# Kernel tuning notes

Hardware: AMD Instinct MI355X
Metric: run time of the kernel (lower is better)

Reference implementation:

```python
import jax, jax.numpy as jnp
import numpy as np

B, SQ, SK, DK, DV = 8, 2048, 2048, 256, 256
EPS = 1e-7  # keras.backend.epsilon()


def setup_inputs() -> dict:
    key = jax.random.key(0)
    kq, kk, kv, km = jax.random.split(key, 4)
    query = jax.random.normal(kq, (B, SQ, DK), dtype=jnp.float32)
    k_ = jax.random.normal(kk, (B, SK, DK), dtype=jnp.float32)
    value = jax.random.normal(kv, (B, SK, DV), dtype=jnp.float32)
    mask = jax.random.uniform(km, (B, SK)) > 0.1
    return {"query": query, "key": k_, "value": value, "mask": mask}


def reference(query, key, value, mask):
    d = query.shape[-1]
    # scores: [B, Sq, Sk]
    e = jnp.einsum('bqd,bkd->bqk', query, key) / jnp.sqrt(jnp.asarray(d, query.dtype))
    # original applies exp(e - max) BEFORE masking (non-standard but faithful)
    e = jnp.exp(e - jnp.max(e, axis=-1, keepdims=True))
    q_len, k_len = query.shape[1], key.shape[1]
    causal = (jnp.arange(k_len)[None, :] <= jnp.arange(q_len)[:, None]).astype(query.dtype)
    e = e * causal[None, :, :]                       # history_only mask
    e = e * mask[:, None, :].astype(query.dtype)     # key padding mask
    a = e / (jnp.sum(e, axis=-1, keepdims=True) + EPS)
    return jnp.einsum('bqk,bkv->bqv', a, value)
```

## Files before the change

### kernel.cpp

```cpp
#include <hip/hip_runtime.h>
#include <hip/hip_bf16.h>

#define B_   8
#define SQ_  2048
#define SK_  2048
#define DK_  256
#define DV_  256

#define KT    32
#define PSTR  40
#define TELEM (KT * DK_)
#define NQB   16

typedef __bf16 bf16x8 __attribute__((ext_vector_type(8)));
typedef float  f32x4  __attribute__((ext_vector_type(4)));

__device__ __forceinline__ void gl_lds16(const void* g, void* l) {
    __builtin_amdgcn_global_load_lds(
        (const __attribute__((address_space(1))) void*)g,
        (__attribute__((address_space(3))) void*)l, 16, 0, 0);
}

__global__ __launch_bounds__(256)
void make_tiles(const float* __restrict__ K, const float* __restrict__ V,
                __bf16* __restrict__ Kt, __bf16* __restrict__ Vt)
{
    const int b = blockIdx.x, t = blockIdx.y;
    {
        __bf16* out = Kt + ((size_t)(b * 64 + t)) * TELEM;
        const float* src = K + ((size_t)(b * SK_ + t * KT)) * DK_;
        #pragma unroll
        for (int it = 0; it < 4; ++it) {
            int ci  = it * 256 + threadIdx.x;
            int dk8 = ci >> 5;
            int key = ci & 31;
            const float* p = src + (size_t)key * DK_ + dk8 * 8;
            float4 f0 = *(const float4*)(p);
            float4 f1 = *(const float4*)(p + 4);
            bf16x8 o;
            o[0] = (__bf16)f0.x; o[1] = (__bf16)f0.y; o[2] = (__bf16)f0.z; o[3] = (__bf16)f0.w;
            o[4] = (__bf16)f1.x; o[5] = (__bf16)f1.y; o[6] = (__bf16)f1.z; o[7] = (__bf16)f1.w;
            *(bf16x8*)(out + (size_t)ci * 8) = o;
        }
    }
    {
        __bf16* out = Vt + ((size_t)(b * 64 + t)) * TELEM;
        const float* src = V + ((size_t)(b * SK_ + t * KT)) * DV_;
        int kc8 = threadIdx.x >> 6;
        int dv4 = threadIdx.x & 63;
        const float* p = src + (size_t)(kc8 * 8) * DV_ + dv4 * 4;
        bf16x8 o0, o1, o2, o3;
        #pragma unroll
        for (int j = 0; j < 8; ++j) {
            float4 f = *(const float4*)(p + (size_t)j * DV_);
            o0[j] = (__bf16)f.x; o1[j] = (__bf16)f.y;
            o2[j] = (__bf16)f.z; o3[j] = (__bf16)f.w;
        }
        __bf16* q = out + (size_t)(kc8 * 256 + dv4 * 4) * 8;
        *(bf16x8*)(q)      = o0;
        *(bf16x8*)(q + 8)  = o1;
        *(bf16x8*)(q + 16) = o2;
        *(bf16x8*)(q + 24) = o3;
    }
}

__global__ __launch_bounds__(256, 2)
void attn_fwd(const float* __restrict__ Qg, const __bf16* __restrict__ Kt,
              const __bf16* __restrict__ Vt, const void* __restrict__ Mv,
              __bf16* __restrict__ Opart, float* __restrict__ Lpart,
              int tpc, int slotcap)
{
    __shared__ __align__(16) __bf16 sK[2][TELEM];
    __shared__ __align__(16) __bf16 sV[2][TELEM];
    __shared__ __align__(16) __bf16 sP[4][32 * PSTR];

    const int tid  = threadIdx.x;
    const int wv   = tid >> 6;
    const int lane = tid & 63;
    const int quad = lane >> 4;
    const int l16  = lane & 15;

    const int b = blockIdx.x;

    int yy = blockIdx.y, qb = 0, s = 0;
    for (int q = NQB - 1; q >= 0; --q) {
        int c = (4 * (q + 1) + tpc - 1) / tpc;
        if (yy < c) { qb = q; s = yy; break; }
        yy -= c;
    }
    const int nt = 4 * (qb + 1);
    const int nc = (nt + tpc - 1) / tpc;
    const int t0 = nt * s / nc;
    const int t1 = nt * (s + 1) / nc;

    const int qrow = qb * 128 + wv * 32;

    const unsigned char* Mb = (const unsigned char*)Mv;
    const int*           Mi = (const int*)Mv;
    int nzb = 0;
    {
        const unsigned int* mw = (const unsigned int*)Mv;
        #pragma unroll
        for (int i = 0; i < 32; ++i) {
            unsigned int w = mw[i];
            nzb += ((w & 0x000000ffu) != 0) + ((w & 0x0000ff00u) != 0)
                 + ((w & 0x00ff0000u) != 0) + ((w & 0xff000000u) != 0);
        }
    }
    const bool mask_byte = (nzb > 40);

    bf16x8 qfrag[2][8];
    #pragma unroll
    for (int rs = 0; rs < 2; ++rs) {
        const float* qp = Qg + ((size_t)(b * SQ_ + qrow + rs * 16 + l16)) * DK_ + quad * 8;
        #pragma unroll
        for (int kt = 0; kt < 8; ++kt) {
            float4 f0 = *(const float4*)(qp + kt * 32);
            float4 f1 = *(const float4*)(qp + kt * 32 + 4);
            bf16x8 q;
            q[0] = (__bf16)f0.x; q[1] = (__bf16)f0.y; q[2] = (__bf16)f0.z; q[3] = (__bf16)f0.w;
            q[4] = (__bf16)f1.x; q[5] = (__bf16)f1.y; q[6] = (__bf16)f1.z; q[7] = (__bf16)f1.w;
            qfrag[rs][kt] = q;
        }
    }

    f32x4 oacc[2][16];
    #pragma unroll
    for (int rs = 0; rs < 2; ++rs)
        #pragma unroll
        for (int v = 0; v < 16; ++v) oacc[rs][v] = (f32x4){0.f, 0.f, 0.f, 0.f};
    float lsum[2][4] = {{0.f,0.f,0.f,0.f},{0.f,0.f,0.f,0.f}};

    const __bf16* Kbase = Kt + (size_t)b * 64 * TELEM;
    const __bf16* Vbase = Vt + (size_t)b * 64 * TELEM;
    const size_t  mbase = (size_t)b * SK_;

    {
        const __bf16* kg = Kbase + (size_t)t0 * TELEM;
        const __bf16* vg = Vbase + (size_t)t0 * TELEM;
        #pragma unroll
        for (int r = 0; r < 4; ++r) {
            int ci = r * 256 + tid;
            gl_lds16(kg + (size_t)ci * 8, (char*)&sK[0][0] + ci * 16);
            gl_lds16(vg + (size_t)ci * 8, (char*)&sV[0][0] + ci * 16);
        }
    }
    __syncthreads();

    int cur = 0;
    for (int t = t0; t < t1; ++t) {
        if (t + 1 < t1) {
            const __bf16* kg = Kbase + (size_t)(t + 1) * TELEM;
            const __bf16* vg = Vbase + (size_t)(t + 1) * TELEM;
            #pragma unroll
            for (int r = 0; r < 4; ++r) {
                int ci = r * 256 + tid;
                gl_lds16(kg + (size_t)ci * 8, (char*)&sK[cur ^ 1][0] + ci * 16);
                gl_lds16(vg + (size_t)ci * 8, (char*)&sV[cur ^ 1][0] + ci * 16);
            }
        }

        const int k0 = t * KT;

        f32x4 s00 = {0.f,0.f,0.f,0.f}, s01 = {0.f,0.f,0.f,0.f};
        f32x4 s10 = {0.f,0.f,0.f,0.f}, s11 = {0.f,0.f,0.f,0.f};
        #pragma unroll
        for (int kt = 0; kt < 8; ++kt) {
            bf16x8 b0 = *(const bf16x8*)&sK[cur][(size_t)((kt * 4 + quad) * 32 + l16)      * 8];
            bf16x8 b1 = *(const bf16x8*)&sK[cur][(size_t)((kt * 4 + quad) * 32 + 16 + l16) * 8];
            s00 = __builtin_amdgcn_mfma_f32_16x16x32_bf16(qfrag[0][kt], b0, s00, 0, 0, 0);
            s01 = __builtin_amdgcn_mfma_f32_16x16x32_bf16(qfrag[0][kt], b1, s01, 0, 0, 0);
            s10 = __builtin_amdgcn_mfma_f32_16x16x32_bf16(qfrag[1][kt], b0, s10, 0, 0, 0);
            s11 = __builtin_amdgcn_mfma_f32_16x16x32_bf16(qfrag[1][kt], b1, s11, 0, 0, 0);
        }

        #pragma unroll
        for (int nf = 0; nf < 2; ++nf) {
            int key = k0 + nf * 16 + l16;
            float mk = mask_byte ? (Mb[mbase + key] ? 1.0f : 0.0f)
                                 : (Mi[mbase + key] ? 1.0f : 0.0f);
            #pragma unroll
            for (int rs = 0; rs < 2; ++rs) {
                f32x4 sv = (rs == 0) ? ((nf == 0) ? s00 : s01)
                                     : ((nf == 0) ? s10 : s11);
                #pragma unroll
                for (int i = 0; i < 4; ++i) {
                    int qr = qrow + rs * 16 + quad * 4 + i;
                    float p = __expf(sv[i] * 0.0625f);
                    p = (key <= qr) ? (p * mk) : 0.0f;
                    lsum[rs][i] += p;
                    sP[wv][(rs * 16 + quad * 4 + i) * PSTR + nf * 16 + l16] = (__bf16)p;
                }
            }
        }
        asm volatile("s_waitcnt lgkmcnt(0)" ::: "memory");
        __builtin_amdgcn_wave_barrier();

        {
            bf16x8 pa0 = *(const bf16x8*)&sP[wv][(l16)      * PSTR + quad * 8];
            bf16x8 pa1 = *(const bf16x8*)&sP[wv][(16 + l16) * PSTR + quad * 8];
            #pragma unroll
            for (int vf = 0; vf < 16; ++vf) {
                bf16x8 bv = *(const bf16x8*)&sV[cur][(size_t)(quad * 256 + vf * 16 + l16) * 8];
                oacc[0][vf] = __builtin_amdgcn_mfma_f32_16x16x32_bf16(pa0, bv, oacc[0][vf], 0, 0, 0);
                oacc[1][vf] = __builtin_amdgcn_mfma_f32_16x16x32_bf16(pa1, bv, oacc[1][vf], 0, 0, 0);
            }
        }

        __syncthreads();
        cur ^= 1;
    }

    const size_t slot = ((size_t)(b * NQB + qb)) * slotcap + s;
    #pragma unroll
    for (int rs = 0; rs < 2; ++rs)
        #pragma unroll
        for (int i = 0; i < 4; ++i) {
            float v = lsum[rs][i];
            v += __shfl_xor(v, 1);
            v += __shfl_xor(v, 2);
            v += __shfl_xor(v, 4);
            v += __shfl_xor(v, 8);
            lsum[rs][i] = v;
        }
    if (l16 == 0) {
        #pragma unroll
        for (int rs = 0; rs < 2; ++rs)
            #pragma unroll
            for (int i = 0; i < 4; ++i)
                Lpart[slot * 128 + wv * 32 + rs * 16 + quad * 4 + i] = lsum[rs][i];
    }
    __bf16* ob = Opart + slot * (size_t)(128 * 256);
    #pragma unroll
    for (int rs = 0; rs < 2; ++rs)
        #pragma unroll
        for (int vf = 0; vf < 16; ++vf)
            #pragma unroll
            for (int i = 0; i < 4; ++i)
                ob[(wv * 32 + rs * 16 + quad * 4 + i) * 256 + vf * 16 + l16]
                    = (__bf16)oacc[rs][vf][i];
}

__global__ __launch_bounds__(512)
void attn_reduce(const __bf16* __restrict__ Opart, const float* __restrict__ Lpart,
                 float* __restrict__ Og, int tpc, int slotcap)
{
    const int b    = blockIdx.x;
    const int y    = blockIdx.y;
    const int qb64 = y >> 1;
    const int half = y & 1;
    const int qb   = qb64 >> 1;
    const int rowbase = (qb64 & 1) * 64;
    const int nt   = 4 * (qb + 1);
    const int chunks = (nt + tpc - 1) / tpc;
    const int tid  = threadIdx.x;
    const int row  = tid >> 3;
    const int cg   = tid & 7;

    const size_t sbase = ((size_t)(b * NQB + qb)) * slotcap;
    float acc[16];
    #pragma unroll
    for (int i = 0; i < 16; ++i) acc[i] = 0.f;
    float ls = 0.f;

    for (int s = 0; s < chunks; ++s) {
        const __bf16* p = Opart + (sbase + s) * (size_t)(128 * 256)
                        + (size_t)(rowbase + row) * 256 + half * 128 + cg * 16;
        bf16x8 x0 = *(const bf16x8*)(p);
        bf16x8 x1 = *(const bf16x8*)(p + 8);
        #pragma unroll
        for (int e = 0; e < 8; ++e) { acc[e] += (float)x0[e]; acc[8 + e] += (float)x1[e]; }
        ls += Lpart[(sbase + s) * 128 + rowbase + row];
    }
    const float inv = 1.0f / (ls + 1e-7f);
    float* op = Og + ((size_t)b * SQ_ + qb64 * 64 + row) * DV_ + half * 128 + cg * 16;
    #pragma unroll
    for (int v = 0; v < 4; ++v) {
        float4 o;
        o.x = acc[v * 4 + 0] * inv; o.y = acc[v * 4 + 1] * inv;
        o.z = acc[v * 4 + 2] * inv; o.w = acc[v * 4 + 3] * inv;
        *(float4*)(op + v * 4) = o;
    }
}

extern "C" void kernel_launch(void* const* d_in, const int* in_sizes, int n_in,
                              void* d_out, int out_size, void* d_ws, size_t ws_size,
                              hipStream_t stream) {
    const float* Q = (const float*)d_in[0];
    const float* K = (const float*)d_in[1];
    const float* V = (const float*)d_in[2];
    const void*  M = d_in[3];
    float* Out = (float*)d_out;

    __bf16* Ktl = (__bf16*)d_ws;
    __bf16* Vtl = Ktl + (size_t)B_ * 64 * TELEM;
    __bf16* Opart = Vtl + (size_t)B_ * 64 * TELEM;

    auto need = [](int slotcap) -> size_t {
        return (size_t)(16 * 1024 * 1024)
             + (size_t)(B_ * NQB) * slotcap * (128 * 256) * 2
             + (size_t)(B_ * NQB) * slotcap * 128 * 4;
    };
    int tpc, slotcap;
    if      (ws_size >= need(8)) { tpc = 10; slotcap = 8; }
    else if (ws_size >= need(4)) { tpc = 16; slotcap = 4; }
    else                         { tpc = 64; slotcap = 1; }
    int nch = 0;
    for (int q = 0; q < NQB; ++q) nch += (4 * (q + 1) + tpc - 1) / tpc;

    float* Lpart = (float*)(Opart + (size_t)(B_ * NQB) * slotcap * (128 * 256));

    make_tiles<<<dim3(B_, 64), dim3(256), 0, stream>>>(K, V, Ktl, Vtl);
    attn_fwd<<<dim3(B_, nch), dim3(256), 0, stream>>>(Q, Ktl, Vtl, M, Opart, Lpart,
                                                      tpc, slotcap);
    attn_reduce<<<dim3(B_, 64), dim3(512), 0, stream>>>(Opart, Lpart, Out, tpc, slotcap);
}
```

Before: 139.8 us.

## Single-buffer K/V tiles in LDS to fit three blocks per CU

The attention kernel drops double-buffered K/V shared-memory tiles for a single buffer. The next tile's async global-to-LDS load now starts after the end-of-iteration barrier, and launch bounds rise to 3 blocks per CU. The goal is higher occupancy, so other blocks hide load latency instead of intra-block prefetch, at the cost of serialising each block's load and compute and tightening the register budget (a risk of spills given the large accumulator array). It also wraps the MFMA loops in s_setprio, batches all loads before the conversions in the tile-conversion kernel, and lowers the keys-per-chunk split from 10 to 8.

After: 235.2 us. 68.3% more time.

```diff
diff --git a/kernel.cpp b/kernel.cpp
--- a/kernel.cpp
+++ b/kernel.cpp
@@ -26,37 +26,49 @@
                 __bf16* __restrict__ Kt, __bf16* __restrict__ Vt)
 {
     const int b = blockIdx.x, t = blockIdx.y;
+    const float* ksrc = K + ((size_t)(b * SK_ + t * KT)) * DK_;
+    const float* vsrc = V + ((size_t)(b * SK_ + t * KT)) * DV_;
+
+    float4 kf[8];
+    #pragma unroll
+    for (int it = 0; it < 4; ++it) {
+        int ci  = it * 256 + threadIdx.x;
+        int dk8 = ci >> 5;
+        int key = ci & 31;
+        const float* p = ksrc + (size_t)key * DK_ + dk8 * 8;
+        kf[it * 2]     = *(const float4*)(p);
+        kf[it * 2 + 1] = *(const float4*)(p + 4);
+    }
+    const int kc8 = threadIdx.x >> 6;
+    const int dv4 = threadIdx.x & 63;
+    float4 vf[8];
     {
-        __bf16* out = Kt + ((size_t)(b * 64 + t)) * TELEM;
-        const float* src = K + ((size_t)(b * SK_ + t * KT)) * DK_;
-        #pragma unroll
-        for (int it = 0; it < 4; ++it) {
-            int ci  = it * 256 + threadIdx.x;
-            int dk8 = ci >> 5;
-            int key = ci & 31;
-            const float* p = src + (size_t)key * DK_ + dk8 * 8;
-            float4 f0 = *(const float4*)(p);
-            float4 f1 = *(const float4*)(p + 4);
-            bf16x8 o;
-            o[0] = (__bf16)f0.x; o[1] = (__bf16)f0.y; o[2] = (__bf16)f0.z; o[3] = (__bf16)f0.w;
-            o[4] = (__bf16)f1.x; o[5] = (__bf16)f1.y; o[6] = (__bf16)f1.z; o[7] = (__bf16)f1.w;
-            *(bf16x8*)(out + (size_t)ci * 8) = o;
-        }
-    }
+        const float* p = vsrc + (size_t)(kc8 * 8) * DV_ + dv4 * 4;
+        #pragma unroll
+        for (int j = 0; j < 8; ++j)
+            vf[j] = *(const float4*)(p + (size_t)j * DV_);
+    }
+
+    __bf16* kout = Kt + ((size_t)(b * 64 + t)) * TELEM;
+    #pragma unroll
+    for (int it = 0; it < 4; ++it) {
+        int ci = it * 256 + threadIdx.x;
+        bf16x8 o;
+        o[0] = (__bf16)kf[it*2].x;   o[1] = (__bf16)kf[it*2].y;
+        o[2] = (__bf16)kf[it*2].z;   o[3] = (__bf16)kf[it*2].w;
+        o[4] = (__bf16)kf[it*2+1].x; o[5] = (__bf16)kf[it*2+1].y;
+        o[6] = (__bf16)kf[it*2+1].z; o[7] = (__bf16)kf[it*2+1].w;
+        *(bf16x8*)(kout + (size_t)ci * 8) = o;
+    }
+    __bf16* vout = Vt + ((size_t)(b * 64 + t)) * TELEM;
     {
-        __bf16* out = Vt + ((size_t)(b * 64 + t)) * TELEM;
-        const float* src = V + ((size_t)(b * SK_ + t * KT)) * DV_;
-        int kc8 = threadIdx.x >> 6;
-        int dv4 = threadIdx.x & 63;
-        const float* p = src + (size_t)(kc8 * 8) * DV_ + dv4 * 4;
         bf16x8 o0, o1, o2, o3;
         #pragma unroll
         for (int j = 0; j < 8; ++j) {
-            float4 f = *(const float4*)(p + (size_t)j * DV_);
-            o0[j] = (__bf16)f.x; o1[j] = (__bf16)f.y;
-            o2[j] = (__bf16)f.z; o3[j] = (__bf16)f.w;
-        }
-        __bf16* q = out + (size_t)(kc8 * 256 + dv4 * 4) * 8;
+            o0[j] = (__bf16)vf[j].x; o1[j] = (__bf16)vf[j].y;
+            o2[j] = (__bf16)vf[j].z; o3[j] = (__bf16)vf[j].w;
+        }
+        __bf16* q = vout + (size_t)(kc8 * 256 + dv4 * 4) * 8;
         *(bf16x8*)(q)      = o0;
         *(bf16x8*)(q + 8)  = o1;
         *(bf16x8*)(q + 16) = o2;
@@ -64,14 +76,14 @@
     }
 }
 
-__global__ __launch_bounds__(256, 2)
+__global__ __launch_bounds__(256, 3)
 void attn_fwd(const float* __restrict__ Qg, const __bf16* __restrict__ Kt,
               const __bf16* __restrict__ Vt, const void* __restrict__ Mv,
               __bf16* __restrict__ Opart, float* __restrict__ Lpart,
               int tpc, int slotcap)
 {
-    __shared__ __align__(16) __bf16 sK[2][TELEM];
-    __shared__ __align__(16) __bf16 sV[2][TELEM];
+    __shared__ __align__(16) __bf16 sK[TELEM];
+    __shared__ __align__(16) __bf16 sV[TELEM];
     __shared__ __align__(16) __bf16 sP[4][32 * PSTR];
 
     const int tid  = threadIdx.x;
@@ -141,38 +153,29 @@
         #pragma unroll
         for (int r = 0; r < 4; ++r) {
             int ci = r * 256 + tid;
-            gl_lds16(kg + (size_t)ci * 8, (char*)&sK[0][0] + ci * 16);
-            gl_lds16(vg + (size_t)ci * 8, (char*)&sV[0][0] + ci * 16);
-        }
-    }
-    __syncthreads();
-
-    int cur = 0;
+            gl_lds16(kg + (size_t)ci * 8, (char*)sK + ci * 16);
+            gl_lds16(vg + (size_t)ci * 8, (char*)sV + ci * 16);
+        }
+    }
+
     for (int t = t0; t < t1; ++t) {
-        if (t + 1 < t1) {
-            const __bf16* kg = Kbase + (size_t)(t + 1) * TELEM;
-            const __bf16* vg = Vbase + (size_t)(t + 1) * TELEM;
-            #pragma unroll
-            for (int r = 0; r < 4; ++r) {
-                int ci = r * 256 + tid;
-                gl_lds16(kg + (size_t)ci * 8, (char*)&sK[cur ^ 1][0] + ci * 16);
-                gl_lds16(vg + (size_t)ci * 8, (char*)&sV[cur ^ 1][0] + ci * 16);
-            }
-        }
+        __syncthreads();
 
         const int k0 = t * KT;
 
         f32x4 s00 = {0.f,0.f,0.f,0.f}, s01 = {0.f,0.f,0.f,0.f};
         f32x4 s10 = {0.f,0.f,0.f,0.f}, s11 = {0.f,0.f,0.f,0.f};
+        __builtin_amdgcn_s_setprio(1);
         #pragma unroll
         for (int kt = 0; kt < 8; ++kt) {
-            bf16x8 b0 = *(const bf16x8*)&sK[cur][(size_t)((kt * 4 + quad) * 32 + l16)      * 8];
-            bf16x8 b1 = *(const bf16x8*)&sK[cur][(size_t)((kt * 4 + quad) * 32 + 16 + l16) * 8];
+            bf16x8 b0 = *(const bf16x8*)&sK[(size_t)((kt * 4 + quad) * 32 + l16)      * 8];
+            bf16x8 b1 = *(const bf16x8*)&sK[(size_t)((kt * 4 + quad) * 32 + 16 + l16) * 8];
             s00 = __builtin_amdgcn_mfma_f32_16x16x32_bf16(qfrag[0][kt], b0, s00, 0, 0, 0);
             s01 = __builtin_amdgcn_mfma_f32_16x16x32_bf16(qfrag[0][kt], b1, s01, 0, 0, 0);
             s10 = __builtin_amdgcn_mfma_f32_16x16x32_bf16(qfrag[1][kt], b0, s10, 0, 0, 0);
             s11 = __builtin_amdgcn_mfma_f32_16x16x32_bf16(qfrag[1][kt], b1, s11, 0, 0, 0);
         }
+        __builtin_amdgcn_s_setprio(0);
 
         #pragma unroll
         for (int nf = 0; nf < 2; ++nf) {
@@ -199,16 +202,27 @@
         {
             bf16x8 pa0 = *(const bf16x8*)&sP[wv][(l16)      * PSTR + quad * 8];
             bf16x8 pa1 = *(const bf16x8*)&sP[wv][(16 + l16) * PSTR + quad * 8];
+            __builtin_amdgcn_s_setprio(1);
             #pragma unroll
             for (int vf = 0; vf < 16; ++vf) {
-                bf16x8 bv = *(const bf16x8*)&sV[cur][(size_t)(quad * 256 + vf * 16 + l16) * 8];
+                bf16x8 bv = *(const bf16x8*)&sV[(size_t)(quad * 256 + vf * 16 + l16) * 8];
                 oacc[0][vf] = __builtin_amdgcn_mfma_f32_16x16x32_bf16(pa0, bv, oacc[0][vf], 0, 0, 0);
                 oacc[1][vf] = __builtin_amdgcn_mfma_f32_16x16x32_bf16(pa1, bv, oacc[1][vf], 0, 0, 0);
             }
+            __builtin_amdgcn_s_setprio(0);
         }
 
         __syncthreads();
-        cur ^= 1;
+        if (t + 1 < t1) {
+            const __bf16* kg = Kbase + (size_t)(t + 1) * TELEM;
+            const __bf16* vg = Vbase + (size_t)(t + 1) * TELEM;
+            #pragma unroll
+            for (int r = 0; r < 4; ++r) {
+                int ci = r * 256 + tid;
+                gl_lds16(kg + (size_t)ci * 8, (char*)sK + ci * 16);
+                gl_lds16(vg + (size_t)ci * 8, (char*)sV + ci * 16);
+            }
+        }
     }
 
     const size_t slot = ((size_t)(b * NQB + qb)) * slotcap + s;
@@ -302,7 +316,7 @@
              + (size_t)(B_ * NQB) * slotcap * 128 * 4;
     };
     int tpc, slotcap;
-    if      (ws_size >= need(8)) { tpc = 10; slotcap = 8; }
+    if      (ws_size >= need(8)) { tpc = 8;  slotcap = 8; }
     else if (ws_size >= need(4)) { tpc = 16; slotcap = 4; }
     else                         { tpc = 64; slotcap = 1; }
     int nch = 0;
```
